# Kernel tuning notes

Hardware: AMD Instinct MI355X
Metric: run time of the kernel (lower is better)

The kernel has to match this reference:

```python
import jax, jax.numpy as jnp
import numpy as np

TAU = 0.1          # contrastive_temperature
EPS = 0.05         # property_epsilon
L_LOCAL_G, L_GLOBAL, L_SC_G, L_LOCAL_SC, G_PROP = 1.0, 0.8, 1.0, 0.8, 0.5
B = 4096
D = 256
NUM_PROPS = 4
N_ATOMS = 131072
N_MOTIFS = 32768


def setup_inputs() -> dict:
    key = jax.random.key(0)
    ks = jax.random.split(key, 10)
    return {
        "emb_g_mole": jax.random.normal(ks[0], (B, D), jnp.float32),
        "emb_g_frag": jax.random.normal(ks[1], (N_ATOMS, D), jnp.float32),
        "emb_sc_mole": jax.random.normal(ks[2], (B, D), jnp.float32),
        "emb_sc_shape": jax.random.normal(ks[3], (N_MOTIFS, D), jnp.float32),
        "emb_motif": jax.random.normal(ks[4], (N_MOTIFS, D), jnp.float32),
        "emb_shape": jax.random.normal(ks[5], (N_MOTIFS, D), jnp.float32),
        # scaled so duplicate rows are the only pairs within EPS (realistic sparse mask)
        "prop_pred": jax.random.normal(ks[6], (B, NUM_PROPS), jnp.float32) * 0.05,
        "prop_target": jax.random.normal(ks[7], (B, NUM_PROPS), jnp.float32) * 0.05,
        "batch_g": jax.random.randint(ks[8], (N_ATOMS,), 0, B, jnp.int32),
        "batch_sc": jax.random.randint(ks[9], (N_MOTIFS,), 0, B, jnp.int32),
    }


def _contrastive(emb, props):
    # SupervisedContrastiveLoss: normalized cosine logits, mask from sqrt(cdist) < eps
    n = emb.shape[0]
    e = emb / jnp.maximum(jnp.linalg.norm(emb, axis=1, keepdims=True), 1e-12)
    logits = jnp.matmul(e, e.T) / TAU                       # [n, n]
    log_probs = jax.nn.log_softmax(logits, axis=1)
    sq = jnp.sum(props * props, axis=1)
    d2 = jnp.maximum(sq[:, None] + sq[None, :] - 2.0 * jnp.matmul(props, props.T), 0.0)
    dd = jnp.sqrt(jnp.sqrt(d2)) + 1e-8                      # cdist(...).sqrt() + 1e-8
    mask = (dd < EPS) & (~jnp.eye(n, dtype=bool))           # fill_diagonal_(0)
    cnt = jnp.sum(mask, axis=1)
    row_loss = -jnp.sum(jnp.where(mask, log_probs, 0.0), axis=1) / jnp.maximum(cnt, 1)
    valid = cnt > 0
    nvalid = jnp.sum(valid)
    loss = jnp.sum(jnp.where(valid, row_loss, 0.0)) / jnp.maximum(nvalid, 1)
    return jnp.where(nvalid > 0, loss, 0.0)


def _frag_alignment(emb_g_frag, emb_motif, batch_g, batch_sc):
    ones_g = jnp.ones((emb_g_frag.shape[0],), emb_g_frag.dtype)
    ones_s = jnp.ones((emb_motif.shape[0],), emb_motif.dtype)
    cnt_g = jax.ops.segment_sum(ones_g, batch_g, num_segments=B)
    cnt_s = jax.ops.segment_sum(ones_s, batch_sc, num_segments=B)
    mean_g = jax.ops.segment_sum(emb_g_frag, batch_g, num_segments=B) / jnp.maximum(cnt_g, 1.0)[:, None]
    mean_s = jax.ops.segment_sum(emb_motif, batch_sc, num_segments=B) / jnp.maximum(cnt_s, 1.0)[:, None]
    norms = jnp.linalg.norm(mean_g - mean_s, axis=1)
    valid = (cnt_g > 0) & (cnt_s > 0)
    batch_size = batch_g.max().astype(emb_g_frag.dtype) + 1.0
    return jnp.sum(jnp.where(valid, norms, 0.0)) / batch_size


def reference(emb_g_mole, emb_g_frag, emb_sc_mole, emb_sc_shape, emb_motif,
              emb_shape, prop_pred, prop_target, batch_g, batch_sc):
    l_local_g = _frag_alignment(emb_g_frag, emb_motif, batch_g, batch_sc)
    combined_emb = jnp.concatenate([emb_g_mole, emb_sc_mole], axis=0)    # [2B, d]
    combined_props = jnp.concatenate([prop_pred, prop_pred], axis=0)      # [2B, p]
    l_contr = _contrastive(combined_emb, combined_props)
    l_global = l_contr          # same inputs in both calls -> identical value
    l_local_sc = l_contr
    l_sc_g = jnp.mean(jnp.linalg.norm(emb_sc_shape - emb_shape, axis=1))  # AlignmentLoss mean
    l_prop = jnp.mean((prop_pred - prop_target) ** 2)                     # MSELoss
    l_hes = (L_LOCAL_G * l_local_g + L_GLOBAL * l_global + L_SC_G * l_sc_g
             + L_LOCAL_SC * l_local_sc + G_PROP * l_prop)
    # stacked: [l_hes, l_local_g, l_global, l_sc_g, l_local_sc, l_prop]
    return jnp.stack([l_hes, l_local_g, l_global, l_sc_g, l_local_sc, l_prop])
```

## Files before the change

### kernel.cpp

```cpp
#include <hip/hip_runtime.h>
#include <hip/hip_bf16.h>
#include <stdint.h>

typedef unsigned short u16;
typedef float f32x4 __attribute__((ext_vector_type(4)));
typedef short s16x8 __attribute__((ext_vector_type(8)));
typedef u16   u16x8 __attribute__((ext_vector_type(8)));
typedef u16   u16x4 __attribute__((ext_vector_type(4)));
typedef uint32_t u32x4 __attribute__((ext_vector_type(4)));

#define B_      4096
#define D_      256
#define NA_     131072
#define NM_     32768
#define N2_     8192
#define THR4    6.2499950e-6f
#define K2E     14.426950408889634f

#define OFF_CNT_G   0u
#define OFF_CNT_S   16384u
#define OFF_CUR_G   32768u
#define OFF_CUR_S   49152u
#define OFF_NB      65536u
#define OFF_SCAL    81920u
#define ZERO_BYTES  98304u
#define OFF_T       98304u
#define OFF_C       131072u
#define OFF_S       163840u
#define OFF_PLIST   196608u
#define OFF_OFFS_G  720896u
#define OFF_OFFS_S  737280u
#define OFF_SORT_G  753664u
#define OFF_SORT_S  1277952u
#define OFF_SP      753664u
#define OFF_E       4947968u
#define WS_NEED     9142272u

__device__ inline float wave_sum(float v) {
#pragma unroll
  for (int m = 1; m < 64; m <<= 1) v += __shfl_xor(v, m, 64);
  return v;
}
__device__ inline int wave_sum_i(int v) {
#pragma unroll
  for (int m = 1; m < 64; m <<= 1) v += __shfl_xor(v, m, 64);
  return v;
}
__device__ inline u16 f2bf(float f) {
  uint32_t u = __float_as_uint(f);
  uint32_t r = (u + 0x7FFFu + ((u >> 16) & 1u)) >> 16;
  return (u16)r;
}
__device__ inline float bf2f(u16 v) { return __uint_as_float(((uint32_t)v) << 16); }

__global__ void k_zero(u32x4* __restrict__ p) {
  u32x4 z = {0u, 0u, 0u, 0u};
  p[blockIdx.x * 256 + threadIdx.x] = z;
}

__global__ void k_count(const int* __restrict__ bg, const int* __restrict__ bs,
                        int* cntg, int* cnts, int* bmax) {
  int i = blockIdx.x * 256 + threadIdx.x;
  int b = -1;
  if (i < NA_) { b = bg[i]; atomicAdd(&cntg[b], 1); }
  if (i < NM_) { atomicAdd(&cnts[bs[i]], 1); }
  int m = b;
#pragma unroll
  for (int k = 1; k < 64; k <<= 1) m = max(m, __shfl_xor(m, k, 64));
  if ((threadIdx.x & 63) == 0 && m >= 0) atomicMax(bmax, m);
}

__global__ void k_scan(const int* __restrict__ cntg, const int* __restrict__ cnts,
                       int* offsg, int* offss, int* curg, int* curs) {
  const int* cnt = blockIdx.x == 0 ? cntg : cnts;
  int* offs = blockIdx.x == 0 ? offsg : offss;
  int* cur  = blockIdx.x == 0 ? curg  : curs;
  __shared__ int ls[256];
  int t = threadIdx.x;
  int v[16]; int s = 0;
#pragma unroll
  for (int k = 0; k < 16; k++) { v[k] = cnt[t * 16 + k]; s += v[k]; }
  ls[t] = s;
  __syncthreads();
  for (int off = 1; off < 256; off <<= 1) {
    int add = (t >= off) ? ls[t - off] : 0;
    __syncthreads();
    ls[t] += add;
    __syncthreads();
  }
  int pre = t ? ls[t - 1] : 0;
#pragma unroll
  for (int k = 0; k < 16; k++) { offs[t * 16 + k] = pre; cur[t * 16 + k] = pre; pre += v[k]; }
}

__global__ void k_scatter(const int* __restrict__ bg, const int* __restrict__ bs,
                          int* curg, int* curs, int* sortg, int* sorts) {
  int i = blockIdx.x * 256 + threadIdx.x;
  if (i < NA_) { int b = bg[i]; sortg[atomicAdd(&curg[b], 1)] = i; }
  if (i < NM_) { int b = bs[i]; sorts[atomicAdd(&curs[b], 1)] = i; }
}

__device__ inline void wave_row_sum(const float* __restrict__ src,
                                    const int* __restrict__ sorted,
                                    int off, int cnt, int lane, f32x4* accs) {
  f32x4 a0 = {0.f,0.f,0.f,0.f}, a1 = a0, a2 = a0, a3 = a0;
  f32x4 a4 = a0, a5 = a0, a6 = a0, a7 = a0;
  for (int base = 0; base < cnt; base += 64) {
    int n = min(cnt - base, 64);
    int idx = (lane < n) ? sorted[off + base + lane] : 0;
    int k = 0;
    for (; k + 7 < n; k += 8) {
      int i0 = __shfl(idx, k,     64), i1 = __shfl(idx, k + 1, 64);
      int i2 = __shfl(idx, k + 2, 64), i3 = __shfl(idx, k + 3, 64);
      int i4 = __shfl(idx, k + 4, 64), i5 = __shfl(idx, k + 5, 64);
      int i6 = __shfl(idx, k + 6, 64), i7 = __shfl(idx, k + 7, 64);
      a0 += *(const f32x4*)(src + (size_t)i0 * D_ + lane * 4);
      a1 += *(const f32x4*)(src + (size_t)i1 * D_ + lane * 4);
      a2 += *(const f32x4*)(src + (size_t)i2 * D_ + lane * 4);
      a3 += *(const f32x4*)(src + (size_t)i3 * D_ + lane * 4);
      a4 += *(const f32x4*)(src + (size_t)i4 * D_ + lane * 4);
      a5 += *(const f32x4*)(src + (size_t)i5 * D_ + lane * 4);
      a6 += *(const f32x4*)(src + (size_t)i6 * D_ + lane * 4);
      a7 += *(const f32x4*)(src + (size_t)i7 * D_ + lane * 4);
    }
    for (; k < n; k++) {
      int i0 = __shfl(idx, k, 64);
      a0 += *(const f32x4*)(src + (size_t)i0 * D_ + lane * 4);
    }
  }
  *accs = ((a0 + a1) + (a2 + a3)) + ((a4 + a5) + (a6 + a7));
}

__global__ __launch_bounds__(256) void k_segmean(
    const float* __restrict__ fg, const float* __restrict__ fm,
    const int* __restrict__ cntg, const int* __restrict__ cnts,
    const int* __restrict__ offsg, const int* __restrict__ offss,
    const int* __restrict__ sortg, const int* __restrict__ sorts,
    float* __restrict__ scal) {
  int t = threadIdx.x, w = t >> 6, lane = t & 63;
  int b = blockIdx.x * 4 + w;
  int cg = cntg[b], cs = cnts[b];
  int og = offsg[b], os = offss[b];

  f32x4 sg, ss;
  wave_row_sum(fg, sortg, og, cg, lane, &sg);
  wave_row_sum(fm, sorts, os, cs, lane, &ss);

  float ig = 1.f / fmaxf((float)cg, 1.f);
  float is = 1.f / fmaxf((float)cs, 1.f);
  float dx = sg.x * ig - ss.x * is, dy = sg.y * ig - ss.y * is;
  float dz = sg.z * ig - ss.z * is, dw = sg.w * ig - ss.w * is;
  float v = wave_sum(dx * dx + dy * dy + dz * dz + dw * dw);

  __shared__ float r2[4];
  if (lane == 0) r2[w] = (cg > 0 && cs > 0) ? sqrtf(v) : 0.f;
  __syncthreads();
  if (t == 0) {
    float s = r2[0] + r2[1] + r2[2] + r2[3];
    if (s != 0.f) atomicAdd(&scal[0], s);
  }
}

__global__ void k_pairs(const float* __restrict__ pp, int* __restrict__ nb,
                        int* __restrict__ plist) {
  int a = blockIdx.x;
  f32x4 pa = *(const f32x4*)(pp + (size_t)a * 4);
  for (int b = threadIdx.x; b < B_; b += 256) {
    f32x4 pb = *(const f32x4*)(pp + (size_t)b * 4);
    float dx = pa.x - pb.x, dy = pa.y - pb.y, dz = pa.z - pb.z, dw = pa.w - pb.w;
    float d2 = dx * dx + dy * dy + dz * dz + dw * dw;
    if (d2 < THR4) {
      int pos = atomicAdd(&nb[a], 1);
      if (pos < 32) plist[a * 32 + pos] = b;
    }
  }
}

__global__ void k_norm(const float* __restrict__ gm, const float* __restrict__ scm,
                       u16* __restrict__ E) {
  int w = threadIdx.x >> 6, lane = threadIdx.x & 63;
  int r = blockIdx.x * 4 + w;
  const float* src = (r < B_) ? gm + (size_t)r * D_ : scm + (size_t)(r - B_) * D_;
  f32x4 v = *(const f32x4*)(src + lane * 4);
  float ss = v.x * v.x + v.y * v.y + v.z * v.z + v.w * v.w;
  ss = wave_sum(ss);
  float inv = 1.f / fmaxf(sqrtf(ss), 1e-12f);
  u16x4 o;
  o.x = f2bf(v.x * inv); o.y = f2bf(v.y * inv);
  o.z = f2bf(v.z * inv); o.w = f2bf(v.w * inv);
  *(u16x4*)(E + (size_t)r * D_ + lane * 4) = o;
}

__global__ __launch_bounds__(256) void k_gemm(const u16* __restrict__ E,
                                              float* __restrict__ SP) {
  __shared__ __align__(16) u16 As[128 * 64];
  __shared__ __align__(16) u16 Bs[128 * 64];

  int t = blockIdx.x;
  int bi = (int)((129.0f - sqrtf(129.0f * 129.0f - 8.0f * (float)t)) * 0.5f);
  while ((bi + 1) * (129 - (bi + 1)) / 2 <= t) bi++;
  while (bi * (129 - bi) / 2 > t) bi--;
  int bj = bi + (t - bi * (129 - bi) / 2);

  int row0 = bi * 128, col0 = bj * 128;
  int tid = threadIdx.x, lane = tid & 63, wid = tid >> 6;
  int wr = wid >> 1, wc = wid & 1;

  f32x4 acc[4][4];
#pragma unroll
  for (int mi = 0; mi < 4; mi++)
#pragma unroll
    for (int ni = 0; ni < 4; ni++) {
      f32x4 z = {0.f, 0.f, 0.f, 0.f};
      acc[mi][ni] = z;
    }

  for (int kc = 0; kc < 4; ++kc) {
    __syncthreads();
#pragma unroll
    for (int p = 0; p < 4; p++) {
      int idx = p * 256 + tid;
      int r = idx >> 3;
      int c16 = idx & 7;
      int cb = c16 * 16;
      int cbs = cb ^ ((r & 7) << 4);
      u16x8 va = *(const u16x8*)(E + (size_t)(row0 + r) * D_ + kc * 64 + (cbs >> 1));
      *(u16x8*)(As + r * 64 + c16 * 8) = va;
      u16x8 vb = *(const u16x8*)(E + (size_t)(col0 + r) * D_ + kc * 64 + (cbs >> 1));
      *(u16x8*)(Bs + r * 64 + c16 * 8) = vb;
    }
    __syncthreads();
#pragma unroll
    for (int kk = 0; kk < 2; ++kk) {
      s16x8 af[4], bfr[4];
#pragma unroll
      for (int mi = 0; mi < 4; mi++) {
        int rA = wr * 64 + mi * 16 + (lane & 15);
        int cbf = kk * 64 + (lane >> 4) * 16;
        int addr = rA * 128 + (cbf ^ ((rA & 7) << 4));
        af[mi] = *(const s16x8*)((const char*)As + addr);
      }
#pragma unroll
      for (int ni = 0; ni < 4; ni++) {
        int rB = wc * 64 + ni * 16 + (lane & 15);
        int cbf = kk * 64 + (lane >> 4) * 16;
        int addr = rB * 128 + (cbf ^ ((rB & 7) << 4));
        bfr[ni] = *(const s16x8*)((const char*)Bs + addr);
      }
#pragma unroll
      for (int mi = 0; mi < 4; mi++)
#pragma unroll
        for (int ni = 0; ni < 4; ni++)
          acc[mi][ni] = __builtin_amdgcn_mfma_f32_16x16x32_bf16(af[mi], bfr[ni], acc[mi][ni], 0, 0, 0);
    }
  }

  int g = lane >> 4, cl = lane & 15;
  int sliceR = bj * 2 + wc;
  float colsum[4] = {0.f, 0.f, 0.f, 0.f};
#pragma unroll
  for (int mi = 0; mi < 4; mi++) {
#pragma unroll
    for (int reg = 0; reg < 4; ++reg) {
      int gi = row0 + wr * 64 + mi * 16 + g * 4 + reg;
      float vs = 0.f;
#pragma unroll
      for (int ni = 0; ni < 4; ni++) {
        float e = exp2f(acc[mi][ni][reg] * K2E - K2E);
        vs += e;
        colsum[ni] += e;
      }
#pragma unroll
      for (int m = 1; m < 16; m <<= 1) vs += __shfl_xor(vs, m, 64);
      if (cl == 0) SP[(size_t)sliceR * N2_ + gi] = vs;
    }
  }
  if (bi != bj) {
    int sliceC = bi * 2 + wr;
#pragma unroll
    for (int ni = 0; ni < 4; ni++) {
      float cs = colsum[ni];
      cs += __shfl_xor(cs, 16, 64);
      cs += __shfl_xor(cs, 32, 64);
      if (g == 0) SP[(size_t)sliceC * N2_ + col0 + wc * 64 + ni * 16 + cl] = cs;
    }
  }
}

__global__ void k_sred(const float* __restrict__ SP, float* __restrict__ S) {
  int gi = blockIdx.x * 256 + threadIdx.x;
  float s = 0.f;
  for (int k = 0; k < 128; k++) s += SP[(size_t)k * N2_ + gi];
  S[gi] = s;
}

__global__ void k_tfix(const u16* __restrict__ E, const int* __restrict__ nb,
                       const int* __restrict__ plist, float* __restrict__ T,
                       int* __restrict__ C) {
  int w = threadIdx.x >> 6, lane = threadIdx.x & 63;
  int i = blockIdx.x * 4 + w;
  int a = i & (B_ - 1);
  int n = min(nb[a], 32);
  u16x4 vi = *(const u16x4*)(E + (size_t)i * D_ + lane * 4);
  float ex = bf2f(vi.x), ey = bf2f(vi.y), ez = bf2f(vi.z), ew = bf2f(vi.w);
  float acc = -(ex * ex + ey * ey + ez * ez + ew * ew);
  for (int k = 0; k < n; k++) {
    int b = plist[a * 32 + k];
    u16x4 v1 = *(const u16x4*)(E + (size_t)b * D_ + lane * 4);
    u16x4 v2 = *(const u16x4*)(E + (size_t)(b + B_) * D_ + lane * 4);
    acc += ex * bf2f(v1.x) + ey * bf2f(v1.y) + ez * bf2f(v1.z) + ew * bf2f(v1.w);
    acc += ex * bf2f(v2.x) + ey * bf2f(v2.y) + ez * bf2f(v2.z) + ew * bf2f(v2.w);
  }
  acc = wave_sum(acc);
  if (lane == 0) { T[i] = 10.0f * acc; C[i] = 2 * n - 1; }
}

__global__ void k_lsc(const float* __restrict__ a, const float* __restrict__ b,
                      float* __restrict__ scal) {
  int w = threadIdx.x >> 6, lane = threadIdx.x & 63;
  int wg = blockIdx.x * 4 + w;
  float acc = 0.f;
  for (int r = wg; r < NM_; r += 8192) {
    f32x4 va = *(const f32x4*)(a + (size_t)r * D_ + lane * 4);
    f32x4 vb = *(const f32x4*)(b + (size_t)r * D_ + lane * 4);
    float dx = va.x - vb.x, dy = va.y - vb.y, dz = va.z - vb.z, dw = va.w - vb.w;
    float ss = wave_sum(dx * dx + dy * dy + dz * dz + dw * dw);
    if (lane == 0) acc += sqrtf(ss);
  }
  __shared__ float red[4];
  if (lane == 0) red[w] = acc;
  __syncthreads();
  if (threadIdx.x == 0) atomicAdd(&scal[1], red[0] + red[1] + red[2] + red[3]);
}

__global__ void k_final(const float* __restrict__ S, const float* __restrict__ T,
                        const int* __restrict__ C, const float* __restrict__ scal,
                        const float* __restrict__ pp, const float* __restrict__ pt,
                        float* __restrict__ out) {
  float sp = 0.f;
  for (int i = threadIdx.x; i < B_ * 4; i += 256) {
    float d = pp[i] - pt[i];
    sp += d * d;
  }
  float rls = 0.f; int nv = 0;
  for (int i = threadIdx.x; i < N2_; i += 256) {
    int ci = C[i];
    if (ci > 0) { rls += (10.0f + logf(S[i])) - T[i] / (float)ci; nv++; }
  }
  rls = wave_sum(rls);
  sp  = wave_sum(sp);
  nv  = wave_sum_i(nv);
  __shared__ float r1[4], r3[4]; __shared__ int r2[4];
  int lane = threadIdx.x & 63, w = threadIdx.x >> 6;
  if (lane == 0) { r1[w] = rls; r2[w] = nv; r3[w] = sp; }
  __syncthreads();
  if (threadIdx.x == 0) {
    float rtot = r1[0] + r1[1] + r1[2] + r1[3];
    int nvt = r2[0] + r2[1] + r2[2] + r2[3];
    float sptot = r3[0] + r3[1] + r3[2] + r3[3];
    float l_contr = nvt > 0 ? rtot / (float)nvt : 0.f;
    int bmax = ((const int*)scal)[3];
    float bs = (float)bmax + 1.0f;
    float l_local_g = scal[0] / bs;
    float l_sc = scal[1] / (float)NM_;
    float l_prop = sptot / (float)(B_ * 4);
    float l_hes = 1.0f * l_local_g + 0.8f * l_contr + 1.0f * l_sc + 0.8f * l_contr + 0.5f * l_prop;
    out[0] = l_hes; out[1] = l_local_g; out[2] = l_contr;
    out[3] = l_sc;  out[4] = l_contr;   out[5] = l_prop;
  }
}

extern "C" void kernel_launch(void* const* d_in, const int* in_sizes, int n_in,
                              void* d_out, int out_size, void* d_ws, size_t ws_size,
                              hipStream_t stream) {
  if (ws_size < WS_NEED) return;
  const float* gm  = (const float*)d_in[0];
  const float* fg  = (const float*)d_in[1];
  const float* scm = (const float*)d_in[2];
  const float* scs = (const float*)d_in[3];
  const float* mot = (const float*)d_in[4];
  const float* shp = (const float*)d_in[5];
  const float* pp  = (const float*)d_in[6];
  const float* pt  = (const float*)d_in[7];
  const int* bg = (const int*)d_in[8];
  const int* bs = (const int*)d_in[9];
  float* out = (float*)d_out;
  char* ws = (char*)d_ws;

  int* cntg  = (int*)(ws + OFF_CNT_G);
  int* cnts  = (int*)(ws + OFF_CNT_S);
  int* curg  = (int*)(ws + OFF_CUR_G);
  int* curs  = (int*)(ws + OFF_CUR_S);
  int* nb    = (int*)(ws + OFF_NB);
  float* scal = (float*)(ws + OFF_SCAL);
  float* T   = (float*)(ws + OFF_T);
  int* C     = (int*)(ws + OFF_C);
  float* S   = (float*)(ws + OFF_S);
  int* plist = (int*)(ws + OFF_PLIST);
  int* offsg = (int*)(ws + OFF_OFFS_G);
  int* offss = (int*)(ws + OFF_OFFS_S);
  int* sortg = (int*)(ws + OFF_SORT_G);
  int* sorts = (int*)(ws + OFF_SORT_S);
  float* SP  = (float*)(ws + OFF_SP);
  u16* E     = (u16*)(ws + OFF_E);

  k_zero<<<24, 256, 0, stream>>>((u32x4*)ws);
  k_count<<<512, 256, 0, stream>>>(bg, bs, cntg, cnts, (int*)scal + 3);
  k_scan<<<2, 256, 0, stream>>>(cntg, cnts, offsg, offss, curg, curs);
  k_scatter<<<512, 256, 0, stream>>>(bg, bs, curg, curs, sortg, sorts);
  k_segmean<<<1024, 256, 0, stream>>>(fg, mot, cntg, cnts, offsg, offss, sortg, sorts, scal);
  k_pairs<<<4096, 256, 0, stream>>>(pp, nb, plist);
  k_norm<<<2048, 256, 0, stream>>>(gm, scm, E);
  k_gemm<<<2080, 256, 0, stream>>>(E, SP);
  k_sred<<<32, 256, 0, stream>>>(SP, S);
  k_tfix<<<2048, 256, 0, stream>>>(E, nb, plist, T, C);
  k_lsc<<<2048, 256, 0, stream>>>(scs, shp, scal);
  k_final<<<1, 256, 0, stream>>>(S, T, C, scal, pp, pt, out);
}
```

Baseline: 230.0 us.

## Fuse independent stage kernels and use direct global-to-LDS loads in GEMM

Merges segment-mean, shape alignment, normalization and pair-finding into one launch, with each range of blocks handling one sub-task. Likewise merges the row-sum reduction and the diagonal/positive-pair fix into a second launch. This removes several kernel launches and lets independent work share the GPU at once. The GEMM tile staging now uses global_load_lds to copy straight into LDS, keeping the same XOR swizzle but computed per lane, which cuts the register round trip. The risk is that block-type divergence within one launch could unbalance scheduling.

```diff
diff --git a/kernel.cpp b/kernel.cpp
--- a/kernel.cpp
+++ b/kernel.cpp
@@ -52,6 +52,12 @@
   return (u16)r;
 }
 __device__ inline float bf2f(u16 v) { return __uint_as_float(((uint32_t)v) << 16); }
+
+__device__ inline void gload16(const u16* __restrict__ g, u16* l) {
+  __builtin_amdgcn_global_load_lds(
+      (const __attribute__((address_space(1))) uint32_t*)g,
+      (__attribute__((address_space(3))) uint32_t*)l, 16, 0, 0);
+}
 
 __global__ void k_zero(u32x4* __restrict__ p) {
   u32x4 z = {0u, 0u, 0u, 0u};
@@ -131,64 +137,75 @@
   *accs = ((a0 + a1) + (a2 + a3)) + ((a4 + a5) + (a6 + a7));
 }
 
-__global__ __launch_bounds__(256) void k_segmean(
+__global__ __launch_bounds__(256) void k_fuse1(
     const float* __restrict__ fg, const float* __restrict__ fm,
     const int* __restrict__ cntg, const int* __restrict__ cnts,
     const int* __restrict__ offsg, const int* __restrict__ offss,
     const int* __restrict__ sortg, const int* __restrict__ sorts,
+    const float* __restrict__ scs, const float* __restrict__ shp,
+    const float* __restrict__ gm, const float* __restrict__ scm,
+    const float* __restrict__ pp,
+    u16* __restrict__ E, int* __restrict__ nb, int* __restrict__ plist,
     float* __restrict__ scal) {
   int t = threadIdx.x, w = t >> 6, lane = t & 63;
-  int b = blockIdx.x * 4 + w;
-  int cg = cntg[b], cs = cnts[b];
-  int og = offsg[b], os = offss[b];
-
-  f32x4 sg, ss;
-  wave_row_sum(fg, sortg, og, cg, lane, &sg);
-  wave_row_sum(fm, sorts, os, cs, lane, &ss);
-
-  float ig = 1.f / fmaxf((float)cg, 1.f);
-  float is = 1.f / fmaxf((float)cs, 1.f);
-  float dx = sg.x * ig - ss.x * is, dy = sg.y * ig - ss.y * is;
-  float dz = sg.z * ig - ss.z * is, dw = sg.w * ig - ss.w * is;
-  float v = wave_sum(dx * dx + dy * dy + dz * dz + dw * dw);
-
-  __shared__ float r2[4];
-  if (lane == 0) r2[w] = (cg > 0 && cs > 0) ? sqrtf(v) : 0.f;
-  __syncthreads();
-  if (t == 0) {
-    float s = r2[0] + r2[1] + r2[2] + r2[3];
-    if (s != 0.f) atomicAdd(&scal[0], s);
-  }
-}
-
-__global__ void k_pairs(const float* __restrict__ pp, int* __restrict__ nb,
-                        int* __restrict__ plist) {
-  int a = blockIdx.x;
-  f32x4 pa = *(const f32x4*)(pp + (size_t)a * 4);
-  for (int b = threadIdx.x; b < B_; b += 256) {
-    f32x4 pb = *(const f32x4*)(pp + (size_t)b * 4);
-    float dx = pa.x - pb.x, dy = pa.y - pb.y, dz = pa.z - pb.z, dw = pa.w - pb.w;
-    float d2 = dx * dx + dy * dy + dz * dz + dw * dw;
-    if (d2 < THR4) {
-      int pos = atomicAdd(&nb[a], 1);
-      if (pos < 32) plist[a * 32 + pos] = b;
-    }
-  }
-}
-
-__global__ void k_norm(const float* __restrict__ gm, const float* __restrict__ scm,
-                       u16* __restrict__ E) {
-  int w = threadIdx.x >> 6, lane = threadIdx.x & 63;
-  int r = blockIdx.x * 4 + w;
-  const float* src = (r < B_) ? gm + (size_t)r * D_ : scm + (size_t)(r - B_) * D_;
-  f32x4 v = *(const f32x4*)(src + lane * 4);
-  float ss = v.x * v.x + v.y * v.y + v.z * v.z + v.w * v.w;
-  ss = wave_sum(ss);
-  float inv = 1.f / fmaxf(sqrtf(ss), 1e-12f);
-  u16x4 o;
-  o.x = f2bf(v.x * inv); o.y = f2bf(v.y * inv);
-  o.z = f2bf(v.z * inv); o.w = f2bf(v.w * inv);
-  *(u16x4*)(E + (size_t)r * D_ + lane * 4) = o;
+  int blk = blockIdx.x;
+  __shared__ float sr4[4];
+
+  if (blk < 1024) {
+    int b = blk * 4 + w;
+    int cg = cntg[b], cs = cnts[b];
+    int og = offsg[b], os = offss[b];
+    f32x4 sg, ss;
+    wave_row_sum(fg, sortg, og, cg, lane, &sg);
+    wave_row_sum(fm, sorts, os, cs, lane, &ss);
+    float ig = 1.f / fmaxf((float)cg, 1.f);
+    float is = 1.f / fmaxf((float)cs, 1.f);
+    float dx = sg.x * ig - ss.x * is, dy = sg.y * ig - ss.y * is;
+    float dz = sg.z * ig - ss.z * is, dw = sg.w * ig - ss.w * is;
+    float v = wave_sum(dx * dx + dy * dy + dz * dz + dw * dw);
+    if (lane == 0) sr4[w] = (cg > 0 && cs > 0) ? sqrtf(v) : 0.f;
+    __syncthreads();
+    if (t == 0) {
+      float s = sr4[0] + sr4[1] + sr4[2] + sr4[3];
+      if (s != 0.f) atomicAdd(&scal[0], s);
+    }
+  } else if (blk < 3072) {
+    int wg = (blk - 1024) * 4 + w;
+    float acc = 0.f;
+    for (int r = wg; r < NM_; r += 8192) {
+      f32x4 va = *(const f32x4*)(scs + (size_t)r * D_ + lane * 4);
+      f32x4 vb = *(const f32x4*)(shp + (size_t)r * D_ + lane * 4);
+      float dx = va.x - vb.x, dy = va.y - vb.y, dz = va.z - vb.z, dw = va.w - vb.w;
+      float ss = wave_sum(dx * dx + dy * dy + dz * dz + dw * dw);
+      if (lane == 0) acc += sqrtf(ss);
+    }
+    if (lane == 0) sr4[w] = acc;
+    __syncthreads();
+    if (t == 0) atomicAdd(&scal[1], sr4[0] + sr4[1] + sr4[2] + sr4[3]);
+  } else if (blk < 5120) {
+    int r = (blk - 3072) * 4 + w;
+    const float* src = (r < B_) ? gm + (size_t)r * D_ : scm + (size_t)(r - B_) * D_;
+    f32x4 v = *(const f32x4*)(src + lane * 4);
+    float ss = v.x * v.x + v.y * v.y + v.z * v.z + v.w * v.w;
+    ss = wave_sum(ss);
+    float inv = 1.f / fmaxf(sqrtf(ss), 1e-12f);
+    u16x4 o;
+    o.x = f2bf(v.x * inv); o.y = f2bf(v.y * inv);
+    o.z = f2bf(v.z * inv); o.w = f2bf(v.w * inv);
+    *(u16x4*)(E + (size_t)r * D_ + lane * 4) = o;
+  } else {
+    int a = blk - 5120;
+    f32x4 pa = *(const f32x4*)(pp + (size_t)a * 4);
+    for (int b = t; b < B_; b += 256) {
+      f32x4 pb = *(const f32x4*)(pp + (size_t)b * 4);
+      float dx = pa.x - pb.x, dy = pa.y - pb.y, dz = pa.z - pb.z, dw = pa.w - pb.w;
+      float d2 = dx * dx + dy * dy + dz * dz + dw * dw;
+      if (d2 < THR4) {
+        int pos = atomicAdd(&nb[a], 1);
+        if (pos < 32) plist[a * 32 + pos] = b;
+      }
+    }
+  }
 }
 
 __global__ __launch_bounds__(256) void k_gemm(const u16* __restrict__ E,
@@ -206,6 +223,9 @@
   int tid = threadIdx.x, lane = tid & 63, wid = tid >> 6;
   int wr = wid >> 1, wc = wid & 1;
 
+  int rsub = lane >> 3;
+  int csw  = (((lane & 7) ^ rsub) << 4) >> 1;
+
   f32x4 acc[4][4];
 #pragma unroll
   for (int mi = 0; mi < 4; mi++)
@@ -218,16 +238,11 @@
   for (int kc = 0; kc < 4; ++kc) {
     __syncthreads();
 #pragma unroll
-    for (int p = 0; p < 4; p++) {
-      int idx = p * 256 + tid;
-      int r = idx >> 3;
-      int c16 = idx & 7;
-      int cb = c16 * 16;
-      int cbs = cb ^ ((r & 7) << 4);
-      u16x8 va = *(const u16x8*)(E + (size_t)(row0 + r) * D_ + kc * 64 + (cbs >> 1));
-      *(u16x8*)(As + r * 64 + c16 * 8) = va;
-      u16x8 vb = *(const u16x8*)(E + (size_t)(col0 + r) * D_ + kc * 64 + (cbs >> 1));
-      *(u16x8*)(Bs + r * 64 + c16 * 8) = vb;
+    for (int it = 0; it < 4; it++) {
+      int s = wid * 4 + it;
+      int r = s * 8 + rsub;
+      gload16(E + (size_t)(row0 + r) * D_ + kc * 64 + csw, As + s * 512);
+      gload16(E + (size_t)(col0 + r) * D_ + kc * 64 + csw, Bs + s * 512);
     }
     __syncthreads();
 #pragma unroll
@@ -287,50 +302,34 @@
   }
 }
 
-__global__ void k_sred(const float* __restrict__ SP, float* __restrict__ S) {
-  int gi = blockIdx.x * 256 + threadIdx.x;
-  float s = 0.f;
-  for (int k = 0; k < 128; k++) s += SP[(size_t)k * N2_ + gi];
-  S[gi] = s;
-}
-
-__global__ void k_tfix(const u16* __restrict__ E, const int* __restrict__ nb,
-                       const int* __restrict__ plist, float* __restrict__ T,
-                       int* __restrict__ C) {
-  int w = threadIdx.x >> 6, lane = threadIdx.x & 63;
-  int i = blockIdx.x * 4 + w;
-  int a = i & (B_ - 1);
-  int n = min(nb[a], 32);
-  u16x4 vi = *(const u16x4*)(E + (size_t)i * D_ + lane * 4);
-  float ex = bf2f(vi.x), ey = bf2f(vi.y), ez = bf2f(vi.z), ew = bf2f(vi.w);
-  float acc = -(ex * ex + ey * ey + ez * ez + ew * ew);
-  for (int k = 0; k < n; k++) {
-    int b = plist[a * 32 + k];
-    u16x4 v1 = *(const u16x4*)(E + (size_t)b * D_ + lane * 4);
-    u16x4 v2 = *(const u16x4*)(E + (size_t)(b + B_) * D_ + lane * 4);
-    acc += ex * bf2f(v1.x) + ey * bf2f(v1.y) + ez * bf2f(v1.z) + ew * bf2f(v1.w);
-    acc += ex * bf2f(v2.x) + ey * bf2f(v2.y) + ez * bf2f(v2.z) + ew * bf2f(v2.w);
-  }
-  acc = wave_sum(acc);
-  if (lane == 0) { T[i] = 10.0f * acc; C[i] = 2 * n - 1; }
-}
-
-__global__ void k_lsc(const float* __restrict__ a, const float* __restrict__ b,
-                      float* __restrict__ scal) {
-  int w = threadIdx.x >> 6, lane = threadIdx.x & 63;
-  int wg = blockIdx.x * 4 + w;
-  float acc = 0.f;
-  for (int r = wg; r < NM_; r += 8192) {
-    f32x4 va = *(const f32x4*)(a + (size_t)r * D_ + lane * 4);
-    f32x4 vb = *(const f32x4*)(b + (size_t)r * D_ + lane * 4);
-    float dx = va.x - vb.x, dy = va.y - vb.y, dz = va.z - vb.z, dw = va.w - vb.w;
-    float ss = wave_sum(dx * dx + dy * dy + dz * dz + dw * dw);
-    if (lane == 0) acc += sqrtf(ss);
-  }
-  __shared__ float red[4];
-  if (lane == 0) red[w] = acc;
-  __syncthreads();
-  if (threadIdx.x == 0) atomicAdd(&scal[1], red[0] + red[1] + red[2] + red[3]);
+__global__ __launch_bounds__(256) void k_fuse2(
+    const float* __restrict__ SP, float* __restrict__ S,
+    const u16* __restrict__ E, const int* __restrict__ nb,
+    const int* __restrict__ plist, float* __restrict__ T, int* __restrict__ C) {
+  int blk = blockIdx.x;
+  if (blk < 32) {
+    int gi = blk * 256 + threadIdx.x;
+    float s = 0.f;
+    for (int k = 0; k < 128; k++) s += SP[(size_t)k * N2_ + gi];
+    S[gi] = s;
+  } else {
+    int w = threadIdx.x >> 6, lane = threadIdx.x & 63;
+    int i = (blk - 32) * 4 + w;
+    int a = i & (B_ - 1);
+    int n = min(nb[a], 32);
+    u16x4 vi = *(const u16x4*)(E + (size_t)i * D_ + lane * 4);
+    float ex = bf2f(vi.x), ey = bf2f(vi.y), ez = bf2f(vi.z), ew = bf2f(vi.w);
+    float acc = -(ex * ex + ey * ey + ez * ez + ew * ew);
+    for (int k = 0; k < n; k++) {
+      int b = plist[a * 32 + k];
+      u16x4 v1 = *(const u16x4*)(E + (size_t)b * D_ + lane * 4);
+      u16x4 v2 = *(const u16x4*)(E + (size_t)(b + B_) * D_ + lane * 4);
+      acc += ex * bf2f(v1.x) + ey * bf2f(v1.y) + ez * bf2f(v1.z) + ew * bf2f(v1.w);
+      acc += ex * bf2f(v2.x) + ey * bf2f(v2.y) + ez * bf2f(v2.z) + ew * bf2f(v2.w);
+    }
+    acc = wave_sum(acc);
+    if (lane == 0) { T[i] = 10.0f * acc; C[i] = 2 * n - 1; }
+  }
 }
 
 __global__ void k_final(const float* __restrict__ S, const float* __restrict__ T,
@@ -408,12 +407,9 @@
   k_count<<<512, 256, 0, stream>>>(bg, bs, cntg, cnts, (int*)scal + 3);
   k_scan<<<2, 256, 0, stream>>>(cntg, cnts, offsg, offss, curg, curs);
   k_scatter<<<512, 256, 0, stream>>>(bg, bs, curg, curs, sortg, sorts);
-  k_segmean<<<1024, 256, 0, stream>>>(fg, mot, cntg, cnts, offsg, offss, sortg, sorts, scal);
-  k_pairs<<<4096, 256, 0, stream>>>(pp, nb, plist);
-  k_norm<<<2048, 256, 0, stream>>>(gm, scm, E);
+  k_fuse1<<<9216, 256, 0, stream>>>(fg, mot, cntg, cnts, offsg, offss, sortg, sorts,
+                                    scs, shp, gm, scm, pp, E, nb, plist, scal);
   k_gemm<<<2080, 256, 0, stream>>>(E, SP);
-  k_sred<<<32, 256, 0, stream>>>(SP, S);
-  k_tfix<<<2048, 256, 0, stream>>>(E, nb, plist, T, C);
-  k_lsc<<<2048, 256, 0, stream>>>(scs, shp, scal);
+  k_fuse2<<<2080, 256, 0, stream>>>(SP, S, E, nb, plist, T, C);
   k_final<<<1, 256, 0, stream>>>(S, T, C, scal, pp, pt, out);
 }
```

Measured after the change: 215.4 us. 6.3% less time.
